# Kernel optimization log

Measured on AMD Instinct MI355X. Metric: run time of the kernel, lower is better.

Reference implementation:

```python
import jax, jax.numpy as jnp
import numpy as np

B, T, N, H = 4096, 128, 128, 128  # batch, timesteps, input_size, encoder_num_hidden
EPS = 1e-5  # BatchNorm1d eps


def setup_inputs() -> dict:
    key = jax.random.key(0)
    ks = jax.random.split(key, 12)
    g = lambda k, shp, s=0.088: jax.random.normal(k, shp, dtype=jnp.float32) * s  # ~1/sqrt(H)
    return {
        "X": jax.random.normal(ks[0], (B, T, N), dtype=jnp.float32),
        "attn_w": g(ks[1], (2 * H + T,)),
        "attn_b": jnp.zeros((), jnp.float32),
        "bn_gamma": jnp.ones((N,), jnp.float32),
        "bn_beta": jnp.zeros((N,), jnp.float32),
        "W_ih0": g(ks[2], (4 * H, N)),
        "W_hh0": g(ks[3], (4 * H, H)),
        "b_ih0": g(ks[4], (4 * H,)),
        "b_hh0": g(ks[5], (4 * H,)),
        "W_ih1": g(ks[6], (4 * H, H)),
        "W_hh1": g(ks[7], (4 * H, H)),
        "b_ih1": g(ks[8], (4 * H,)),
        "b_hh1": g(ks[9], (4 * H,)),
    }


def _lstm_cell(x, h, c, W_ih, W_hh, b):
    # torch gate order: i, f, g, o
    gates = x @ W_ih.T + h @ W_hh.T + b  # (B, 4H)
    i, f, gg, o = jnp.split(gates, 4, axis=-1)
    c_new = jax.nn.sigmoid(f) * c + jax.nn.sigmoid(i) * jnp.tanh(gg)
    h_new = jax.nn.sigmoid(o) * jnp.tanh(c_new)
    return h_new, c_new


def reference(X, attn_w, attn_b, bn_gamma, bn_beta,
              W_ih0, W_hh0, b_ih0, b_hh0, W_ih1, W_hh1, b_ih1, b_hh1):
    # Attention input per step is cat(h_top repeat, s_top repeat, X^T) -> Linear(2H+T -> 1).
    # The X^T contribution is time-invariant; precompute it once.
    w_h, w_s, w_x = attn_w[:H], attn_w[H:2 * H], attn_w[2 * H:]
    Xp = jnp.transpose(X, (0, 2, 1))            # (B, N, T) driving-series view
    score_x = Xp @ w_x + attn_b                 # (B, N)
    b0 = b_ih0 + b_hh0
    b1 = b_ih1 + b_hh1

    def step(carry, x_t):
        h0, c0, h1, c1 = carry                  # layer0/layer1 hidden & cell (B, H)
        # h_n[-1], s_n[-1] are broadcast identically over all N features
        scores = score_x + (h1 @ w_h)[:, None] + (c1 @ w_s)[:, None]  # (B, N)
        alpha = jax.nn.softmax(scores, axis=1)
        x_tilde = alpha * x_t                   # (B, N)
        # BatchNorm1d in training mode: batch statistics over dim 0
        mean = jnp.mean(x_tilde, axis=0)
        var = jnp.var(x_tilde, axis=0)
        xb = (x_tilde - mean) * jax.lax.rsqrt(var + EPS) * bn_gamma + bn_beta
        # 2-layer LSTM single step (dropout inactive in eval)
        h0n, c0n = _lstm_cell(xb, h0, c0, W_ih0, W_hh0, b0)
        h1n, c1n = _lstm_cell(h0n, h1, c1, W_ih1, W_hh1, b1)
        return (h0n, c0n, h1n, c1n), (x_tilde, h1n)

    zeros = jnp.zeros((B, H), X.dtype)
    init = (zeros, zeros, zeros, zeros)
    Xt = jnp.transpose(X, (1, 0, 2))            # (T, B, N) for scan
    _, (xt_seq, he_seq) = jax.lax.scan(step, init, Xt)
    X_tilde = jnp.transpose(xt_seq, (1, 0, 2))   # (B, T, N)
    X_encoded = jnp.transpose(he_seq, (1, 0, 2)) # (B, T, H)
    return X_tilde, X_encoded
```

## Files before the change

kernel.cpp:

```cpp
#include <hip/hip_runtime.h>
#include <cstdint>
#include <cstddef>

#define B_ 4096
#define T_ 128
#define N_ 128
#define H_ 128
#define G4_ 512
#define KC_ 256
#define EPS_ 1e-5f

#define RPB_ 16
#define NB_ 256
#define W0K_ 128
#define W0P_ 136

typedef _Float16 f16x8 __attribute__((ext_vector_type(8)));
typedef _Float16 f16x4 __attribute__((ext_vector_type(4)));
typedef float f32x4 __attribute__((ext_vector_type(4)));

__device__ __forceinline__ float sigm_(float x) { return 1.f / (1.f + __expf(-x)); }
__device__ __forceinline__ float tanh_(float x) {
  float ax = fabsf(x);
  float e = __expf(-2.f * ax);
  float t = (1.f - e) / (1.f + e);
  return copysignf(t, x);
}

__global__ void k0_prep(const float* __restrict__ Wih0, const float* __restrict__ Whh0,
                        const float* __restrict__ bih0, const float* __restrict__ bhh0,
                        const float* __restrict__ Wih1, const float* __restrict__ Whh1,
                        const float* __restrict__ bih1, const float* __restrict__ bhh1,
                        _Float16* __restrict__ Wpack, float* __restrict__ bpack,
                        float* __restrict__ sumb, float* __restrict__ sqb) {
  int idx = blockIdx.x * blockDim.x + threadIdx.x;
  if (idx < 2 * G4_ * KC_) {
    int k = idx & (KC_ - 1);
    int j = (idx >> 8) & (G4_ - 1);
    int l = idx >> 17;
    const float* Wih = l ? Wih1 : Wih0;
    const float* Whh = l ? Whh1 : Whh0;
    float v = (k < N_) ? Wih[j * N_ + k] : Whh[j * N_ + (k - N_)];
    Wpack[idx] = (_Float16)v;
  }
  if (idx < 2 * G4_) {
    int j = idx & (G4_ - 1);
    bpack[idx] = (idx >> 9) ? (bih1[j] + bhh1[j]) : (bih0[j] + bhh0[j]);
  }
  if (idx < T_ * N_) { sumb[idx] = 0.f; sqb[idx] = 0.f; }
}

__global__ void k1_alpha(const float* __restrict__ X, const float* __restrict__ attn_w,
                         const float* __restrict__ attn_b, float* __restrict__ alpha) {
  __shared__ float wx[T_];
  __shared__ float red[4];
  int b = blockIdx.x;
  int n = threadIdx.x;
  wx[n] = attn_w[2 * H_ + n];
  __syncthreads();
  const float* xp = X + (size_t)b * T_ * N_ + n;
  float s = 0.f;
#pragma unroll 8
  for (int t = 0; t < T_; ++t) s = fmaf(xp[t * N_], wx[t], s);
  s += attn_b[0];
  float m = s;
#pragma unroll
  for (int off = 32; off >= 1; off >>= 1) m = fmaxf(m, __shfl_xor(m, off));
  if ((n & 63) == 0) red[n >> 6] = m;
  __syncthreads();
  m = fmaxf(red[0], red[1]);
  float e = __expf(s - m);
  float sm = e;
#pragma unroll
  for (int off = 32; off >= 1; off >>= 1) sm += __shfl_xor(sm, off);
  if ((n & 63) == 0) red[2 + (n >> 6)] = sm;
  __syncthreads();
  sm = red[2] + red[3];
  alpha[b * N_ + n] = e / sm;
}

__global__ void k2_xtilde(const float* __restrict__ X, const float* __restrict__ alpha,
                          float* __restrict__ out0, float* __restrict__ sumb,
                          float* __restrict__ sqb) {
  int t = blockIdx.x;
  int chunk = blockIdx.y;
  int n = threadIdx.x & (N_ - 1);
  int bi = threadIdx.x >> 7;
  float s = 0.f, q = 0.f;
  for (int it = 0; it < 128; ++it) {
    int b = (chunk << 8) + (it << 1) + bi;
    float a = alpha[b * N_ + n];
    size_t off = ((size_t)b * T_ + t) * N_ + n;
    float v = a * X[off];
    out0[off] = v;
    s += v;
    q += v * v;
  }
  __shared__ float ps[2][N_], pq[2][N_];
  ps[bi][n] = s;
  pq[bi][n] = q;
  __syncthreads();
  if (bi == 0) {
    atomicAdd(&sumb[t * N_ + n], ps[0][n] + ps[1][n]);
    atomicAdd(&sqb[t * N_ + n], pq[0][n] + pq[1][n]);
  }
}

__global__ void k3_finalize(const float* __restrict__ sumb, const float* __restrict__ sqb,
                            const float* __restrict__ gamma, const float* __restrict__ beta,
                            float* __restrict__ scale, float* __restrict__ shift) {
  int i = blockIdx.x * blockDim.x + threadIdx.x;
  if (i >= T_ * N_) return;
  int n = i & (N_ - 1);
  float mean = sumb[i] * (1.f / B_);
  float var = sqb[i] * (1.f / B_) - mean * mean;
  float rstd = rsqrtf(var + EPS_);
  float g = gamma[n];
  scale[i] = rstd * g;
  shift[i] = beta[n] - mean * rstd * g;
}

__global__ __launch_bounds__(512, 2) void k4_recur(
    const float* __restrict__ xt , const _Float16* __restrict__ Wpack,
    const float* __restrict__ bpack, const float* __restrict__ scale,
    const float* __restrict__ shift, float* __restrict__ out1) {
  __shared__ _Float16 W0l[G4_][W0P_];
  __shared__ _Float16 A0[RPB_][264];
  __shared__ _Float16 A1[RPB_][264];

  const int tid = threadIdx.x;
  const int w = tid >> 6;
  const int lane = tid & 63;
  const int quad = lane >> 4;
  const int l16 = lane & 15;
  const int nb = blockIdx.x;
  const int col = (w << 4) + l16;

  {
    const _Float16* src = Wpack + (size_t)tid * KC_;
#pragma unroll
    for (int kk = 0; kk < W0K_; kk += 8)
      *(f16x8*)&W0l[tid][kk] = *(const f16x8*)&src[kk];
  }

  f16x8 w1[4][8];
#pragma unroll
  for (int g = 0; g < 4; ++g) {
    const _Float16* src = Wpack + (size_t)(G4_ + (g << 7) + col) * KC_ + (quad << 3);
#pragma unroll
    for (int kb = 0; kb < 8; ++kb) w1[g][kb] = *(const f16x8*)&src[kb << 5];
  }

  float bia0[4], bia1[4];
#pragma unroll
  for (int g = 0; g < 4; ++g) {
    bia0[g] = bpack[(g << 7) + col];
    bia1[g] = bpack[G4_ + (g << 7) + col];
  }

  float c0[4], c1[4];
#pragma unroll
  for (int e = 0; e < 4; ++e) { c0[e] = 0.f; c1[e] = 0.f; }

  const int srow = tid >> 5;
  const int scol = (tid & 31) << 2;
  const size_t browbase = (size_t)(nb * RPB_ + srow) * T_;

  {
    f32x4 xv = *(const f32x4*)(xt + (browbase + 0) * N_ + scol);
    f32x4 sc = *(const f32x4*)(scale + scol);
    f32x4 sh = *(const f32x4*)(shift + scol);
    f16x4 hv;
#pragma unroll
    for (int e = 0; e < 4; ++e) hv[e] = (_Float16)fmaf(xv[e], sc[e], sh[e]);
    *(f16x4*)&A0[srow][scol] = hv;
    f16x4 z = {};
    *(f16x4*)&A0[srow][N_ + scol] = z;
    *(f16x4*)&A1[srow][N_ + scol] = z;
  }
  __syncthreads();

  for (int t = 0; t < T_; ++t) {
    f32x4 xn = {};
    if (t + 1 < T_) xn = *(const f32x4*)(xt + (browbase + t + 1) * N_ + scol);

    f32x4 acc[4] = {};
#pragma unroll
    for (int kb = 0; kb < 8; ++kb) {
      f16x8 a = *(const f16x8*)&A0[l16][(kb << 5) + (quad << 3)];
      if (kb < 4) {
#pragma unroll
        for (int g = 0; g < 4; ++g) {
          f16x8 bf = *(const f16x8*)&W0l[(g << 7) + col][(kb << 5) + (quad << 3)];
          acc[g] = __builtin_amdgcn_mfma_f32_16x16x32_f16(a, bf, acc[g], 0, 0, 0);
        }
      } else {
#pragma unroll
        for (int g = 0; g < 4; ++g) {
          f16x8 bf = *(const f16x8*)(Wpack + (size_t)((g << 7) + col) * KC_ +
                                     (kb << 5) + (quad << 3));
          acc[g] = __builtin_amdgcn_mfma_f32_16x16x32_f16(a, bf, acc[g], 0, 0, 0);
        }
      }
    }

    _Float16 h0h[4];
#pragma unroll
    for (int e = 0; e < 4; ++e) {
      float ig = acc[0][e] + bia0[0];
      float fg = acc[1][e] + bia0[1];
      float gg = acc[2][e] + bia0[2];
      float og = acc[3][e] + bia0[3];
      float cn = sigm_(fg) * c0[e] + sigm_(ig) * tanh_(gg);
      c0[e] = cn;
      h0h[e] = (_Float16)(sigm_(og) * tanh_(cn));
    }
    __syncthreads();
#pragma unroll
    for (int e = 0; e < 4; ++e) {
      A0[(quad << 2) + e][N_ + col] = h0h[e];
      A1[(quad << 2) + e][col] = h0h[e];
    }
    __syncthreads();

    f32x4 acc1[4] = {};
#pragma unroll
    for (int kb = 0; kb < 8; ++kb) {
      f16x8 a = *(const f16x8*)&A1[l16][(kb << 5) + (quad << 3)];
#pragma unroll
      for (int g = 0; g < 4; ++g)
        acc1[g] = __builtin_amdgcn_mfma_f32_16x16x32_f16(a, w1[g][kb], acc1[g], 0, 0, 0);
    }

    _Float16 h1h[4];
#pragma unroll
    for (int e = 0; e < 4; ++e) {
      float ig = acc1[0][e] + bia1[0];
      float fg = acc1[1][e] + bia1[1];
      float gg = acc1[2][e] + bia1[2];
      float og = acc1[3][e] + bia1[3];
      float cn = sigm_(fg) * c1[e] + sigm_(ig) * tanh_(gg);
      c1[e] = cn;
      float hn = sigm_(og) * tanh_(cn);
      h1h[e] = (_Float16)hn;
      out1[((size_t)(nb * RPB_ + (quad << 2) + e) * T_ + t) * H_ + col] = hn;
    }
    __syncthreads();
#pragma unroll
    for (int e = 0; e < 4; ++e)
      A1[(quad << 2) + e][N_ + col] = h1h[e];
    if (t + 1 < T_) {
      f32x4 sc = *(const f32x4*)(scale + (t + 1) * N_ + scol);
      f32x4 sh = *(const f32x4*)(shift + (t + 1) * N_ + scol);
      f16x4 hv;
#pragma unroll
      for (int e = 0; e < 4; ++e) hv[e] = (_Float16)fmaf(xn[e], sc[e], sh[e]);
      *(f16x4*)&A0[srow][scol] = hv;
    }
    __syncthreads();
  }
}

extern "C" void kernel_launch(void* const* d_in, const int* in_sizes, int n_in,
                              void* d_out, int out_size, void* d_ws, size_t ws_size,
                              hipStream_t stream) {
  const float* X = (const float*)d_in[0];
  const float* attnw = (const float*)d_in[1];
  const float* attnb = (const float*)d_in[2];
  const float* gamma = (const float*)d_in[3];
  const float* beta = (const float*)d_in[4];
  const float* Wih0 = (const float*)d_in[5];
  const float* Whh0 = (const float*)d_in[6];
  const float* bih0 = (const float*)d_in[7];
  const float* bhh0 = (const float*)d_in[8];
  const float* Wih1 = (const float*)d_in[9];
  const float* Whh1 = (const float*)d_in[10];
  const float* bih1 = (const float*)d_in[11];
  const float* bhh1 = (const float*)d_in[12];

  float* out0 = (float*)d_out;
  float* out1 = out0 + (size_t)B_ * T_ * N_;

  float* ws = (float*)d_ws;
  float* alpha = ws;
  float* sumb = alpha + (size_t)B_ * N_;
  float* sqb = sumb + T_ * N_;
  float* scale = sqb + T_ * N_;
  float* shift = scale + T_ * N_;
  float* bpack = shift + T_ * N_;
  _Float16* Wpack = (_Float16*)(bpack + 2 * G4_);

  k0_prep<<<1024, 256, 0, stream>>>(Wih0, Whh0, bih0, bhh0, Wih1, Whh1, bih1, bhh1,
                                    Wpack, bpack, sumb, sqb);
  k1_alpha<<<B_, 128, 0, stream>>>(X, attnw, attnb, alpha);
  k2_xtilde<<<dim3(T_, 16), 256, 0, stream>>>(X, alpha, out0, sumb, sqb);
  k3_finalize<<<64, 256, 0, stream>>>(sumb, sqb, gamma, beta, scale, shift);
  k4_recur<<<NB_, 512, 0, stream>>>(out0, Wpack, bpack, scale, shift, out1);
}
```

Measured before the change: 1.437 ms.

## Vectorize attention kernels and double-buffer LSTM recurrence state with swizzled weights

k1_alpha now stages the whole X row block in shared memory with 256 threads and splits the time reduction across two halves. k2_xtilde uses float4 loads and stores, with an 8-row partial reduction before the atomics. The recurrence kernel splits its activation buffers into separate XB/H0/H1 tiles, double-buffering H0 and H1 so one __syncthreads per step can be dropped. It XOR-swizzles the shared W0 layout against bank conflicts and preloads A fragments and global W-hh0 fragments before issuing the MFMAs. The risks are added register pressure from holding the preloaded fragments, and the asm barrier trick used to keep the global loads inside the loop.

```diff
diff --git a/kernel.cpp b/kernel.cpp
--- a/kernel.cpp
+++ b/kernel.cpp
@@ -13,7 +13,7 @@
 #define RPB_ 16
 #define NB_ 256
 #define W0K_ 128
-#define W0P_ 136
+#define APAD_ 136
 
 typedef _Float16 f16x8 __attribute__((ext_vector_type(8)));
 typedef _Float16 f16x4 __attribute__((ext_vector_type(4)));
@@ -52,31 +52,45 @@
 
 __global__ void k1_alpha(const float* __restrict__ X, const float* __restrict__ attn_w,
                          const float* __restrict__ attn_b, float* __restrict__ alpha) {
+  __shared__ float xs[T_ * N_];
   __shared__ float wx[T_];
-  __shared__ float red[4];
+  __shared__ float ps[2][N_];
+  __shared__ float red[8];
   int b = blockIdx.x;
-  int n = threadIdx.x;
-  wx[n] = attn_w[2 * H_ + n];
-  __syncthreads();
-  const float* xp = X + (size_t)b * T_ * N_ + n;
+  int tid = threadIdx.x;
+  if (tid < T_) wx[tid] = attn_w[2 * H_ + tid];
+  const float* xb = X + (size_t)b * T_ * N_;
+#pragma unroll
+  for (int i = 0; i < 16; ++i) {
+    int fi = ((i << 8) + tid) << 2;
+    *(f32x4*)&xs[fi] = *(const f32x4*)&xb[fi];
+  }
+  __syncthreads();
+  int n = tid & 127, hf = tid >> 7;
   float s = 0.f;
+  {
+    int t0 = hf << 6;
 #pragma unroll 8
-  for (int t = 0; t < T_; ++t) s = fmaf(xp[t * N_], wx[t], s);
-  s += attn_b[0];
+    for (int tt = 0; tt < 64; ++tt) s = fmaf(xs[(t0 + tt) * N_ + n], wx[t0 + tt], s);
+  }
+  ps[hf][n] = s;
+  __syncthreads();
+  s = ps[0][n] + ps[1][n] + attn_b[0];
   float m = s;
 #pragma unroll
   for (int off = 32; off >= 1; off >>= 1) m = fmaxf(m, __shfl_xor(m, off));
-  if ((n & 63) == 0) red[n >> 6] = m;
+  int wv = tid >> 6;
+  if ((tid & 63) == 0) red[wv] = m;
   __syncthreads();
   m = fmaxf(red[0], red[1]);
   float e = __expf(s - m);
   float sm = e;
 #pragma unroll
   for (int off = 32; off >= 1; off >>= 1) sm += __shfl_xor(sm, off);
-  if ((n & 63) == 0) red[2 + (n >> 6)] = sm;
-  __syncthreads();
-  sm = red[2] + red[3];
-  alpha[b * N_ + n] = e / sm;
+  if ((tid & 63) == 0) red[4 + wv] = sm;
+  __syncthreads();
+  sm = red[4] + red[5];
+  if (hf == 0) alpha[b * N_ + n] = e / sm;
 }
 
 __global__ void k2_xtilde(const float* __restrict__ X, const float* __restrict__ alpha,
@@ -84,25 +98,32 @@
                           float* __restrict__ sqb) {
   int t = blockIdx.x;
   int chunk = blockIdx.y;
-  int n = threadIdx.x & (N_ - 1);
-  int bi = threadIdx.x >> 7;
-  float s = 0.f, q = 0.f;
-  for (int it = 0; it < 128; ++it) {
-    int b = (chunk << 8) + (it << 1) + bi;
-    float a = alpha[b * N_ + n];
-    size_t off = ((size_t)b * T_ + t) * N_ + n;
-    float v = a * X[off];
-    out0[off] = v;
-    s += v;
-    q += v * v;
-  }
-  __shared__ float ps[2][N_], pq[2][N_];
-  ps[bi][n] = s;
-  pq[bi][n] = q;
-  __syncthreads();
-  if (bi == 0) {
-    atomicAdd(&sumb[t * N_ + n], ps[0][n] + ps[1][n]);
-    atomicAdd(&sqb[t * N_ + n], pq[0][n] + pq[1][n]);
+  int tid = threadIdx.x;
+  int c = (tid & 31) << 2;
+  int r = tid >> 5;
+  f32x4 s4 = {}, q4 = {};
+  for (int it = 0; it < 32; ++it) {
+    int b = (chunk << 8) + (it << 3) + r;
+    f32x4 a4 = *(const f32x4*)&alpha[b * N_ + c];
+    size_t off = ((size_t)b * T_ + t) * N_ + c;
+    f32x4 x4 = *(const f32x4*)&X[off];
+    f32x4 v;
+#pragma unroll
+    for (int e = 0; e < 4; ++e) v[e] = a4[e] * x4[e];
+    *(f32x4*)&out0[off] = v;
+#pragma unroll
+    for (int e = 0; e < 4; ++e) { s4[e] += v[e]; q4[e] += v[e] * v[e]; }
+  }
+  __shared__ float ps[8][N_], pq[8][N_];
+  *(f32x4*)&ps[r][c] = s4;
+  *(f32x4*)&pq[r][c] = q4;
+  __syncthreads();
+  if (tid < N_) {
+    float s = 0.f, q = 0.f;
+#pragma unroll
+    for (int rr = 0; rr < 8; ++rr) { s += ps[rr][tid]; q += pq[rr][tid]; }
+    atomicAdd(&sumb[t * N_ + tid], s);
+    atomicAdd(&sqb[t * N_ + tid], q);
   }
 }
 
@@ -124,9 +145,11 @@
     const float* __restrict__ xt , const _Float16* __restrict__ Wpack,
     const float* __restrict__ bpack, const float* __restrict__ scale,
     const float* __restrict__ shift, float* __restrict__ out1) {
-  __shared__ _Float16 W0l[G4_][W0P_];
-  __shared__ _Float16 A0[RPB_][264];
-  __shared__ _Float16 A1[RPB_][264];
+  __shared__ _Float16 W0l[G4_ * 128];
+  __shared__ _Float16 XB[RPB_][APAD_];
+  __shared__ _Float16 H0A[2][RPB_][APAD_];
+  __shared__ _Float16 H0B[RPB_][APAD_];
+  __shared__ _Float16 H1[2][RPB_][APAD_];
 
   const int tid = threadIdx.x;
   const int w = tid >> 6;
@@ -138,9 +161,11 @@
 
   {
     const _Float16* src = Wpack + (size_t)tid * KC_;
-#pragma unroll
-    for (int kk = 0; kk < W0K_; kk += 8)
-      *(f16x8*)&W0l[tid][kk] = *(const f16x8*)&src[kk];
+    char* dst = (char*)W0l + tid * 256;
+    const int sw = (tid & 7) << 4;
+#pragma unroll
+    for (int o = 0; o < 256; o += 16)
+      *(f16x8*)(dst + (o ^ sw)) = *(const f16x8*)((const char*)src + o);
   }
 
   f16x8 w1[4][8];
@@ -148,7 +173,8 @@
   for (int g = 0; g < 4; ++g) {
     const _Float16* src = Wpack + (size_t)(G4_ + (g << 7) + col) * KC_ + (quad << 3);
 #pragma unroll
-    for (int kb = 0; kb < 8; ++kb) w1[g][kb] = *(const f16x8*)&src[kb << 5];
+    for (int kb = 0; kb < 8; ++kb)
+      w1[g][kb] = *(volatile const f16x8*)&src[kb << 5];
   }
 
   float bia0[4], bia1[4];
@@ -162,46 +188,63 @@
 #pragma unroll
   for (int e = 0; e < 4; ++e) { c0[e] = 0.f; c1[e] = 0.f; }
 
-  const int srow = tid >> 5;
-  const int scol = (tid & 31) << 2;
-  const size_t browbase = (size_t)(nb * RPB_ + srow) * T_;
+  const int sr = tid >> 5;
+  const int sc = (tid & 31) << 2;
+  const size_t browbase = (size_t)(nb * RPB_ + sr) * T_;
 
   {
-    f32x4 xv = *(const f32x4*)(xt + (browbase + 0) * N_ + scol);
-    f32x4 sc = *(const f32x4*)(scale + scol);
-    f32x4 sh = *(const f32x4*)(shift + scol);
+    f32x4 xv = *(const f32x4*)(xt + (browbase + 0) * N_ + sc);
+    f32x4 s4 = *(const f32x4*)(scale + sc);
+    f32x4 h4 = *(const f32x4*)(shift + sc);
     f16x4 hv;
 #pragma unroll
-    for (int e = 0; e < 4; ++e) hv[e] = (_Float16)fmaf(xv[e], sc[e], sh[e]);
-    *(f16x4*)&A0[srow][scol] = hv;
+    for (int e = 0; e < 4; ++e) hv[e] = (_Float16)fmaf(xv[e], s4[e], h4[e]);
+    *(f16x4*)&XB[sr][sc] = hv;
     f16x4 z = {};
-    *(f16x4*)&A0[srow][N_ + scol] = z;
-    *(f16x4*)&A1[srow][N_ + scol] = z;
-  }
-  __syncthreads();
+    *(f16x4*)&H0A[0][sr][sc] = z;
+    *(f16x4*)&H1[0][sr][sc] = z;
+  }
+  __syncthreads();
+
+  const int swr = (l16 & 7) << 4;
 
   for (int t = 0; t < T_; ++t) {
+    const int cb = t & 1, cbn = cb ^ 1;
+
+    int z = 0;
+    asm volatile("" : "+v"(z));
+
     f32x4 xn = {};
-    if (t + 1 < T_) xn = *(const f32x4*)(xt + (browbase + t + 1) * N_ + scol);
-
+    if (t + 1 < T_) xn = *(const f32x4*)(xt + (browbase + t + 1) * N_ + sc);
+
+    f16x8 a[8];
+#pragma unroll
+    for (int kb = 0; kb < 4; ++kb) {
+      a[kb] = *(const f16x8*)&XB[l16][(kb << 5) + (quad << 3)];
+      a[4 + kb] = *(const f16x8*)&H0A[cb][l16][(kb << 5) + (quad << 3)];
+    }
     f32x4 acc[4] = {};
 #pragma unroll
-    for (int kb = 0; kb < 8; ++kb) {
-      f16x8 a = *(const f16x8*)&A0[l16][(kb << 5) + (quad << 3)];
-      if (kb < 4) {
-#pragma unroll
-        for (int g = 0; g < 4; ++g) {
-          f16x8 bf = *(const f16x8*)&W0l[(g << 7) + col][(kb << 5) + (quad << 3)];
-          acc[g] = __builtin_amdgcn_mfma_f32_16x16x32_f16(a, bf, acc[g], 0, 0, 0);
-        }
-      } else {
-#pragma unroll
-        for (int g = 0; g < 4; ++g) {
-          f16x8 bf = *(const f16x8*)(Wpack + (size_t)((g << 7) + col) * KC_ +
-                                     (kb << 5) + (quad << 3));
-          acc[g] = __builtin_amdgcn_mfma_f32_16x16x32_f16(a, bf, acc[g], 0, 0, 0);
-        }
-      }
+    for (int g = 0; g < 4; ++g) {
+      const _Float16* wpg =
+          Wpack + (size_t)((g << 7) + col) * KC_ + W0K_ + (quad << 3) + z;
+      f16x8 b4 = *(const f16x8*)&wpg[0];
+      f16x8 b5 = *(const f16x8*)&wpg[32];
+      f16x8 b6 = *(const f16x8*)&wpg[64];
+      f16x8 b7 = *(const f16x8*)&wpg[96];
+      const char* wr = (const char*)W0l + (((g << 7) + col) << 8);
+      f16x8 b0 = *(const f16x8*)(wr + (((0 << 6) | (quad << 4)) ^ swr));
+      f16x8 b1 = *(const f16x8*)(wr + (((1 << 6) | (quad << 4)) ^ swr));
+      f16x8 b2 = *(const f16x8*)(wr + (((2 << 6) | (quad << 4)) ^ swr));
+      f16x8 b3 = *(const f16x8*)(wr + (((3 << 6) | (quad << 4)) ^ swr));
+      acc[g] = __builtin_amdgcn_mfma_f32_16x16x32_f16(a[0], b0, acc[g], 0, 0, 0);
+      acc[g] = __builtin_amdgcn_mfma_f32_16x16x32_f16(a[1], b1, acc[g], 0, 0, 0);
+      acc[g] = __builtin_amdgcn_mfma_f32_16x16x32_f16(a[2], b2, acc[g], 0, 0, 0);
+      acc[g] = __builtin_amdgcn_mfma_f32_16x16x32_f16(a[3], b3, acc[g], 0, 0, 0);
+      acc[g] = __builtin_amdgcn_mfma_f32_16x16x32_f16(a[4], b4, acc[g], 0, 0, 0);
+      acc[g] = __builtin_amdgcn_mfma_f32_16x16x32_f16(a[5], b5, acc[g], 0, 0, 0);
+      acc[g] = __builtin_amdgcn_mfma_f32_16x16x32_f16(a[6], b6, acc[g], 0, 0, 0);
+      acc[g] = __builtin_amdgcn_mfma_f32_16x16x32_f16(a[7], b7, acc[g], 0, 0, 0);
     }
 
     _Float16 h0h[4];
@@ -215,21 +258,30 @@
       c0[e] = cn;
       h0h[e] = (_Float16)(sigm_(og) * tanh_(cn));
     }
+#pragma unroll
+    for (int e = 0; e < 4; ++e) {
+      H0A[cbn][(quad << 2) + e][col] = h0h[e];
+      H0B[(quad << 2) + e][col] = h0h[e];
+    }
     __syncthreads();
-#pragma unroll
-    for (int e = 0; e < 4; ++e) {
-      A0[(quad << 2) + e][N_ + col] = h0h[e];
-      A1[(quad << 2) + e][col] = h0h[e];
-    }
-    __syncthreads();
-
+
+    f16x8 a1[8];
+#pragma unroll
+    for (int kb = 0; kb < 4; ++kb) {
+      a1[kb] = *(const f16x8*)&H0B[l16][(kb << 5) + (quad << 3)];
+      a1[4 + kb] = *(const f16x8*)&H1[cb][l16][(kb << 5) + (quad << 3)];
+    }
     f32x4 acc1[4] = {};
 #pragma unroll
-    for (int kb = 0; kb < 8; ++kb) {
-      f16x8 a = *(const f16x8*)&A1[l16][(kb << 5) + (quad << 3)];
-#pragma unroll
-      for (int g = 0; g < 4; ++g)
-        acc1[g] = __builtin_amdgcn_mfma_f32_16x16x32_f16(a, w1[g][kb], acc1[g], 0, 0, 0);
+    for (int g = 0; g < 4; ++g) {
+      acc1[g] = __builtin_amdgcn_mfma_f32_16x16x32_f16(a1[0], w1[g][0], acc1[g], 0, 0, 0);
+      acc1[g] = __builtin_amdgcn_mfma_f32_16x16x32_f16(a1[1], w1[g][1], acc1[g], 0, 0, 0);
+      acc1[g] = __builtin_amdgcn_mfma_f32_16x16x32_f16(a1[2], w1[g][2], acc1[g], 0, 0, 0);
+      acc1[g] = __builtin_amdgcn_mfma_f32_16x16x32_f16(a1[3], w1[g][3], acc1[g], 0, 0, 0);
+      acc1[g] = __builtin_amdgcn_mfma_f32_16x16x32_f16(a1[4], w1[g][4], acc1[g], 0, 0, 0);
+      acc1[g] = __builtin_amdgcn_mfma_f32_16x16x32_f16(a1[5], w1[g][5], acc1[g], 0, 0, 0);
+      acc1[g] = __builtin_amdgcn_mfma_f32_16x16x32_f16(a1[6], w1[g][6], acc1[g], 0, 0, 0);
+      acc1[g] = __builtin_amdgcn_mfma_f32_16x16x32_f16(a1[7], w1[g][7], acc1[g], 0, 0, 0);
     }
 
     _Float16 h1h[4];
@@ -245,17 +297,16 @@
       h1h[e] = (_Float16)hn;
       out1[((size_t)(nb * RPB_ + (quad << 2) + e) * T_ + t) * H_ + col] = hn;
     }
-    __syncthreads();
 #pragma unroll
     for (int e = 0; e < 4; ++e)
-      A1[(quad << 2) + e][N_ + col] = h1h[e];
+      H1[cbn][(quad << 2) + e][col] = h1h[e];
     if (t + 1 < T_) {
-      f32x4 sc = *(const f32x4*)(scale + (t + 1) * N_ + scol);
-      f32x4 sh = *(const f32x4*)(shift + (t + 1) * N_ + scol);
+      f32x4 s4 = *(const f32x4*)(scale + (t + 1) * N_ + sc);
+      f32x4 h4 = *(const f32x4*)(shift + (t + 1) * N_ + sc);
       f16x4 hv;
 #pragma unroll
-      for (int e = 0; e < 4; ++e) hv[e] = (_Float16)fmaf(xn[e], sc[e], sh[e]);
-      *(f16x4*)&A0[srow][scol] = hv;
+      for (int e = 0; e < 4; ++e) hv[e] = (_Float16)fmaf(xn[e], s4[e], h4[e]);
+      *(f16x4*)&XB[sr][sc] = hv;
     }
     __syncthreads();
   }
@@ -292,7 +343,7 @@
 
   k0_prep<<<1024, 256, 0, stream>>>(Wih0, Whh0, bih0, bhh0, Wih1, Whh1, bih1, bhh1,
                                     Wpack, bpack, sumb, sqb);
-  k1_alpha<<<B_, 128, 0, stream>>>(X, attnw, attnb, alpha);
+  k1_alpha<<<B_, 256, 0, stream>>>(X, attnw, attnb, alpha);
   k2_xtilde<<<dim3(T_, 16), 256, 0, stream>>>(X, alpha, out0, sumb, sqb);
   k3_finalize<<<64, 256, 0, stream>>>(sumb, sqb, gamma, beta, scale, shift);
   k4_recur<<<NB_, 512, 0, stream>>>(out0, Wpack, bpack, scale, shift, out1);
```

New measurement: 1.748 ms. +21.7%, slower.
